# Kernel tuning notes

Measured on AMD Instinct MI355X. Metric: run time of the kernel, lower is better.

The kernel has to match this reference:

```python
import jax, jax.numpy as jnp
import numpy as np


def setup_inputs() -> dict:
    key = jax.random.key(0)
    k1, k2 = jax.random.split(key)
    N, P, D = 65536, 512, 256
    feature_vectors = jax.random.normal(k1, (N, D), dtype=jnp.float32)
    prototypes = jax.random.normal(k2, (P, D), dtype=jnp.float32)
    return {"feature_vectors": feature_vectors, "prototypes": prototypes}


def reference(feature_vectors, prototypes):
    # squared norms
    feat_sq = jnp.sum(feature_vectors * feature_vectors, axis=1)   # [N]
    proto_sq = jnp.sum(prototypes * prototypes, axis=1)            # [P]
    # cross term: [N, P]
    cross = feature_vectors @ prototypes.T
    # dists_to_protos: [N, P] = |f|^2 + |p|^2 - 2 f.p
    dists_to_protos = feat_sq[:, None] + proto_sq[None, :] - 2.0 * cross
    # dists_to_latents: [P, N] (original does a second matmul; it's the transpose)
    dists_to_latents = proto_sq[:, None] + feat_sq[None, :] - 2.0 * cross.T
    return (dists_to_protos, dists_to_latents)
```

## Files before the change

### kernel.cpp

```cpp
#include <hip/hip_runtime.h>
#include <hip/hip_bf16.h>


#define DD 256
#define PP 512
#define BN 64
#define TP 36

typedef short bf16x8 __attribute__((ext_vector_type(8)));
typedef float f32x16 __attribute__((ext_vector_type(16)));
typedef float f32x4 __attribute__((ext_vector_type(4)));
typedef unsigned short u16x4 __attribute__((ext_vector_type(4)));

__device__ __forceinline__ unsigned short f2bf(float f) {
    unsigned int u = __builtin_bit_cast(unsigned int, f);
    u = (u + 0x7fffu + ((u >> 16) & 1u)) >> 16;
    return (unsigned short)u;
}

__global__ __launch_bounds__(256) void proto_prep(const float* __restrict__ proto,
                                                  unsigned short* __restrict__ bw,
                                                  float* __restrict__ psq) {
    const int w = threadIdx.x >> 6, lane = threadIdx.x & 63;
    const int row = blockIdx.x * 4 + w;
    const f32x4 f = *(const f32x4*)(proto + (size_t)row * DD + lane * 4);
    u16x4 u;
    u.x = f2bf(f.x); u.y = f2bf(f.y); u.z = f2bf(f.z); u.w = f2bf(f.w);
    *(u16x4*)(bw + (size_t)row * DD + lane * 4) = u;
    float part = f.x * f.x + f.y * f.y + f.z * f.z + f.w * f.w;
    for (int o = 32; o > 0; o >>= 1) part += __shfl_xor(part, o, 64);
    if (lane == 0) psq[row] = part;
}

__global__ __launch_bounds__(512, 4) void proto_dist(
        const float* __restrict__ feat,
        const unsigned short* __restrict__ bw,
        const float* __restrict__ psq,
        float* __restrict__ out0,
        float* __restrict__ out1,
        int N) {
    __shared__ unsigned char S[8 * 32 * TP * 4];
    __shared__ float fsq[BN];
    unsigned short* A_lds = (unsigned short*)S;

    const int tid = threadIdx.x;
    const int w = tid >> 6, lane = tid & 63;
    const int n0 = blockIdx.x * BN;

    #pragma unroll
    for (int i = 0; i < 8; ++i) {
        const int row = i * 8 + w;
        const f32x4 f = __builtin_nontemporal_load(
            (const f32x4*)(feat + (size_t)(n0 + row) * DD + lane * 4));
        u16x4 u;
        u.x = f2bf(f.x); u.y = f2bf(f.y); u.z = f2bf(f.z); u.w = f2bf(f.w);
        *(u16x4*)&A_lds[row * 264 + lane * 4] = u;
        float part = f.x * f.x + f.y * f.y + f.z * f.z + f.w * f.w;
        for (int o = 32; o > 0; o >>= 1) part += __shfl_xor(part, o, 64);
        if (lane == 0) fsq[row] = part;
    }
    __syncthreads();

    const int r = w & 1;
    const int g = w >> 1;
    const int colbase = g * 128;
    const int l31 = lane & 31;
    const int hi = lane >> 5;

    f32x16 acc[4];
    #pragma unroll
    for (int t = 0; t < 4; ++t)
        #pragma unroll
        for (int e = 0; e < 16; ++e) acc[t][e] = 0.0f;

    const unsigned short* arow = &A_lds[(32 * r + l31) * 264 + hi * 8];
    const unsigned short* bbase = bw + (size_t)(colbase + l31) * DD + hi * 8;

    #pragma unroll 2
    for (int k0 = 0; k0 < DD; k0 += 16) {
        const bf16x8 a = *(const bf16x8*)(arow + k0);
        #pragma unroll
        for (int t = 0; t < 4; ++t) {
            const bf16x8 b = *(const bf16x8*)(bbase + (size_t)(32 * t) * DD + k0);
            acc[t] = __builtin_amdgcn_mfma_f32_32x32x16_bf16(a, b, acc[t], 0, 0, 0);
        }
    }

    __syncthreads();
    float* trans = ((float*)S) + w * (32 * TP);

    float fsq_q[4][4];
    #pragma unroll
    for (int q = 0; q < 4; ++q)
        #pragma unroll
        for (int e = 0; e < 4; ++e)
            fsq_q[q][e] = fsq[32 * r + e + 8 * q + 4 * hi];

    float* out0_base = out0 + (size_t)(n0 + 32 * r) * PP;

    #pragma unroll
    for (int t = 0; t < 4; ++t) {
        const int p = colbase + 32 * t + l31;
        const float psq_v = psq[p];
        #pragma unroll
        for (int q = 0; q < 4; ++q) {
            f32x4 d;
            #pragma unroll
            for (int e = 0; e < 4; ++e) {
                const int reg = 4 * q + e;
                const int n_l = e + 8 * q + 4 * hi;
                const float dist = fsq_q[q][e] + psq_v - 2.0f * acc[t][reg];
                d[e] = dist;
                __builtin_nontemporal_store(dist, out0_base + (size_t)n_l * PP + p);
            }
            *(f32x4*)&trans[l31 * TP + 8 * q + 4 * hi] = d;
        }
        #pragma unroll
        for (int j = 0; j < 4; ++j) {
            const int p_row = j * 8 + (lane >> 3);
            const int n_off = (lane & 7) * 4;
            const f32x4 v = *(const f32x4*)&trans[p_row * TP + n_off];
            __builtin_nontemporal_store(v,
                (f32x4*)(out1 + (size_t)(colbase + 32 * t + p_row) * N
                               + (n0 + 32 * r + n_off)));
        }
    }
}

extern "C" void kernel_launch(void* const* d_in, const int* in_sizes, int n_in,
                              void* d_out, int out_size, void* d_ws, size_t ws_size,
                              hipStream_t stream) {
    const float* feat = (const float*)d_in[0];
    const float* proto = (const float*)d_in[1];
    const int N = in_sizes[0] / DD;

    unsigned short* bw = (unsigned short*)d_ws;
    float* psq = (float*)((char*)d_ws + (size_t)PP * DD * 2);

    float* out0 = (float*)d_out;
    float* out1 = out0 + (size_t)N * PP;

    proto_prep<<<PP / 4, 256, 0, stream>>>(proto, bw, psq);
    proto_dist<<<N / BN, 512, 0, stream>>>(feat, bw, psq, out0, out1, N);
}
```

Before: 357.3 us.

## Pre-swizzle prototype bf16 into MFMA fragment order and split LDS buffers

The prep kernel now writes prototypes in bf16 in the exact per-lane MFMA B-fragment order, so each wave's B load in the main loop becomes one contiguous 16-byte-per-lane coalesced load instead of strided row reads. The A tile in LDS gets its own buffer with a wider row pitch (280), and the transpose scratch gets a separate buffer. That separation removes the __syncthreads between the matmul and the epilogue. fsq values are also read as vector loads. The cost is more LDS per block, which may reduce occupancy. The kernel is dominated by output writes, so the gain is likely small.

After: 320.5 us. 10.3% less time.

```diff
diff --git a/kernel.cpp b/kernel.cpp
--- a/kernel.cpp
+++ b/kernel.cpp
@@ -5,6 +5,7 @@
 #define DD 256
 #define PP 512
 #define BN 64
+#define AP 280
 #define TP 36
 
 typedef short bf16x8 __attribute__((ext_vector_type(8)));
@@ -19,17 +20,30 @@
 }
 
 __global__ __launch_bounds__(256) void proto_prep(const float* __restrict__ proto,
-                                                  unsigned short* __restrict__ bw,
+                                                  unsigned short* __restrict__ bwf,
                                                   float* __restrict__ psq) {
     const int w = threadIdx.x >> 6, lane = threadIdx.x & 63;
-    const int row = blockIdx.x * 4 + w;
-    const f32x4 f = *(const f32x4*)(proto + (size_t)row * DD + lane * 4);
-    u16x4 u;
-    u.x = f2bf(f.x); u.y = f2bf(f.y); u.z = f2bf(f.z); u.w = f2bf(f.w);
-    *(u16x4*)(bw + (size_t)row * DD + lane * 4) = u;
-    float part = f.x * f.x + f.y * f.y + f.z * f.z + f.w * f.w;
-    for (int o = 32; o > 0; o >>= 1) part += __shfl_xor(part, o, 64);
-    if (lane == 0) psq[row] = part;
+    const int l31 = lane & 31, hf = lane >> 5;
+    const int row = blockIdx.x * 8 + w * 2 + hf;
+    const int oct = l31;
+    const float* src = proto + (size_t)row * DD + oct * 8;
+    const f32x4 f0 = *(const f32x4*)(src);
+    const f32x4 f1 = *(const f32x4*)(src + 4);
+    bf16x8 b;
+    b[0] = (short)f2bf(f0.x); b[1] = (short)f2bf(f0.y);
+    b[2] = (short)f2bf(f0.z); b[3] = (short)f2bf(f0.w);
+    b[4] = (short)f2bf(f1.x); b[5] = (short)f2bf(f1.y);
+    b[6] = (short)f2bf(f1.z); b[7] = (short)f2bf(f1.w);
+    const int tile = row >> 5;
+    const int kk = oct >> 1;
+    const int fl = ((oct & 1) << 5) | (row & 31);
+    *(bf16x8*)(bwf + ((size_t)(tile * 16 + kk) * 64 + fl) * 8) = b;
+
+    float part = f0.x * f0.x + f0.y * f0.y + f0.z * f0.z + f0.w * f0.w
+               + f1.x * f1.x + f1.y * f1.y + f1.z * f1.z + f1.w * f1.w;
+    #pragma unroll
+    for (int o = 16; o > 0; o >>= 1) part += __shfl_xor(part, o, 64);
+    if (l31 == 0) psq[row] = part;
 }
 
 __global__ __launch_bounds__(512, 4) void proto_dist(
@@ -39,9 +53,9 @@
         float* __restrict__ out0,
         float* __restrict__ out1,
         int N) {
-    __shared__ unsigned char S[8 * 32 * TP * 4];
+    __shared__ unsigned short A_lds[BN * AP];
+    __shared__ float Strans[8 * 32 * TP];
     __shared__ float fsq[BN];
-    unsigned short* A_lds = (unsigned short*)S;
 
     const int tid = threadIdx.x;
     const int w = tid >> 6, lane = tid & 63;
@@ -54,7 +68,7 @@
             (const f32x4*)(feat + (size_t)(n0 + row) * DD + lane * 4));
         u16x4 u;
         u.x = f2bf(f.x); u.y = f2bf(f.y); u.z = f2bf(f.z); u.w = f2bf(f.w);
-        *(u16x4*)&A_lds[row * 264 + lane * 4] = u;
+        *(u16x4*)&A_lds[row * AP + lane * 4] = u;
         float part = f.x * f.x + f.y * f.y + f.z * f.z + f.w * f.w;
         for (int o = 32; o > 0; o >>= 1) part += __shfl_xor(part, o, 64);
         if (lane == 0) fsq[row] = part;
@@ -63,9 +77,12 @@
 
     const int r = w & 1;
     const int g = w >> 1;
-    const int colbase = g * 128;
+    const int colT = g * 128;
     const int l31 = lane & 31;
     const int hi = lane >> 5;
+
+    const unsigned short* arow = &A_lds[(32 * r + l31) * AP + hi * 8];
+    const unsigned short* bwf_w = bw + (size_t)g * 4 * 16 * 512;
 
     f32x16 acc[4];
     #pragma unroll
@@ -73,43 +90,35 @@
         #pragma unroll
         for (int e = 0; e < 16; ++e) acc[t][e] = 0.0f;
 
-    const unsigned short* arow = &A_lds[(32 * r + l31) * 264 + hi * 8];
-    const unsigned short* bbase = bw + (size_t)(colbase + l31) * DD + hi * 8;
-
     #pragma unroll 2
-    for (int k0 = 0; k0 < DD; k0 += 16) {
-        const bf16x8 a = *(const bf16x8*)(arow + k0);
+    for (int kk = 0; kk < 16; ++kk) {
+        const bf16x8 a = *(const bf16x8*)(arow + kk * 16);
         #pragma unroll
         for (int t = 0; t < 4; ++t) {
-            const bf16x8 b = *(const bf16x8*)(bbase + (size_t)(32 * t) * DD + k0);
+            const bf16x8 b = *(const bf16x8*)(bwf_w + ((t * 16 + kk) * 64 + lane) * 8);
             acc[t] = __builtin_amdgcn_mfma_f32_32x32x16_bf16(a, b, acc[t], 0, 0, 0);
         }
     }
 
-    __syncthreads();
-    float* trans = ((float*)S) + w * (32 * TP);
-
-    float fsq_q[4][4];
+    f32x4 fsq_q[4];
     #pragma unroll
     for (int q = 0; q < 4; ++q)
-        #pragma unroll
-        for (int e = 0; e < 4; ++e)
-            fsq_q[q][e] = fsq[32 * r + e + 8 * q + 4 * hi];
+        fsq_q[q] = *(const f32x4*)&fsq[32 * r + 8 * q + 4 * hi];
 
+    float* trans = Strans + w * (32 * TP);
     float* out0_base = out0 + (size_t)(n0 + 32 * r) * PP;
 
     #pragma unroll
     for (int t = 0; t < 4; ++t) {
-        const int p = colbase + 32 * t + l31;
+        const int p = colT + 32 * t + l31;
         const float psq_v = psq[p];
         #pragma unroll
         for (int q = 0; q < 4; ++q) {
             f32x4 d;
             #pragma unroll
             for (int e = 0; e < 4; ++e) {
-                const int reg = 4 * q + e;
                 const int n_l = e + 8 * q + 4 * hi;
-                const float dist = fsq_q[q][e] + psq_v - 2.0f * acc[t][reg];
+                const float dist = fsq_q[q][e] + psq_v - 2.0f * acc[t][4 * q + e];
                 d[e] = dist;
                 __builtin_nontemporal_store(dist, out0_base + (size_t)n_l * PP + p);
             }
@@ -121,7 +130,7 @@
             const int n_off = (lane & 7) * 4;
             const f32x4 v = *(const f32x4*)&trans[p_row * TP + n_off];
             __builtin_nontemporal_store(v,
-                (f32x4*)(out1 + (size_t)(colbase + 32 * t + p_row) * N
+                (f32x4*)(out1 + (size_t)(colT + 32 * t + p_row) * N
                                + (n0 + 32 * r + n_off)));
         }
     }
@@ -140,6 +149,6 @@
     float* out0 = (float*)d_out;
     float* out1 = out0 + (size_t)N * PP;
 
-    proto_prep<<<PP / 4, 256, 0, stream>>>(proto, bw, psq);
+    proto_prep<<<PP / 8, 256, 0, stream>>>(proto, bw, psq);
     proto_dist<<<N / BN, 512, 0, stream>>>(feat, bw, psq, out0, out1, N);
 }
```
